# Optimization experiments

Hardware: AMD Instinct MI355X
Metric: run time of the kernel (lower is better)

## Reference

```python
import jax, jax.numpy as jnp
import numpy as np

D_MODEL = 1024
H = 16
DK = 64
DV = 64
EPS = 1e-5


def setup_inputs() -> dict:
    key = jax.random.key(0)
    ks = jax.random.split(key, 12)
    B, NQ, NK = 4, 2048, 2048
    std = 0.001  # init.normal_(weight, std=0.001), biases zero
    return {
        "queries": jax.random.normal(ks[0], (B, NQ, D_MODEL), jnp.float32),
        "keys": jax.random.normal(ks[1], (B, NK, D_MODEL), jnp.float32),
        "values": jax.random.normal(ks[2], (B, NK, D_MODEL), jnp.float32),
        "attention_mask": jnp.ones((B, NK), jnp.int32),  # 1 = keep
        "Wq": jax.random.normal(ks[3], (D_MODEL, H * DK), jnp.float32) * std,
        "bq": jnp.zeros((H * DK,), jnp.float32),
        "Wk": jax.random.normal(ks[4], (D_MODEL, H * DK), jnp.float32) * std,
        "bk": jnp.zeros((H * DK,), jnp.float32),
        "Wv": jax.random.normal(ks[5], (D_MODEL, H * DV), jnp.float32) * std,
        "bv": jnp.zeros((H * DV,), jnp.float32),
        "Wo": jax.random.normal(ks[6], (H * DV, D_MODEL), jnp.float32) * std,
        "bo": jnp.zeros((D_MODEL,), jnp.float32),
        "gamma": jnp.ones((D_MODEL,), jnp.float32),
        "beta": jnp.zeros((D_MODEL,), jnp.float32),
    }


def reference(queries, keys, values, attention_mask, Wq, bq, Wk, bk, Wv, bv, Wo, bo, gamma, beta):
    b, nq, _ = queries.shape
    nk = keys.shape[1]
    q = (queries @ Wq + bq).reshape(b, nq, H, DK)   # (b, nq, h, dk)
    k = (keys @ Wk + bk).reshape(b, nk, H, DK)      # (b, nk, h, dk)
    v = (values @ Wv + bv).reshape(b, nk, H, DV)    # (b, nk, h, dv)
    scale = 1.0 / np.sqrt(DK).astype(np.float32)
    att = jnp.einsum('bqhd,bkhd->bhqk', q, k) * scale  # (b, h, nq, nk)
    mask = attention_mask[:, None, None, :].astype(bool)
    att = jnp.where(mask, att, -jnp.inf)
    att = jax.nn.softmax(att, axis=-1)
    # dropout is identity at inference
    out = jnp.einsum('bhqk,bkhd->bqhd', att, v).reshape(b, nq, H * DV)
    out = out @ Wo + bo
    x = out + queries  # residual
    mean = jnp.mean(x, axis=-1, keepdims=True)
    var = jnp.mean(jnp.square(x - mean), axis=-1, keepdims=True)
    return gamma * (x - mean) * jax.lax.rsqrt(var + EPS) + beta
```

## Files before the change

### kernel.cpp

```cpp
#include <hip/hip_runtime.h>

typedef __bf16 bf16x8 __attribute__((ext_vector_type(8)));
typedef __bf16 bf16x4 __attribute__((ext_vector_type(4)));
typedef float f32x4 __attribute__((ext_vector_type(4)));
typedef unsigned short u16;

#if __has_builtin(__builtin_amdgcn_exp2f)
#define EXP2(x) __builtin_amdgcn_exp2f(x)
#else
#define EXP2(x) exp2f(x)
#endif

__device__ __forceinline__ float bf2f(u16 u){
    union { unsigned int i; float f; } x; x.i = ((unsigned int)u) << 16; return x.f;
}
__device__ __forceinline__ u16 f2bf(float f){
    union { float f; unsigned int i; } x; x.f = f;
    unsigned int r = x.i + 0x7fff + ((x.i >> 16) & 1);
    return (u16)(r >> 16);
}
__device__ __forceinline__ int4 cvt8(const float4 a, const float4 b){
    union { u16 h[8]; int4 v; } u;
    u.h[0] = f2bf(a.x); u.h[1] = f2bf(a.y); u.h[2] = f2bf(a.z); u.h[3] = f2bf(a.w);
    u.h[4] = f2bf(b.x); u.h[5] = f2bf(b.y); u.h[6] = f2bf(b.z); u.h[7] = f2bf(b.w);
    return u.v;
}
__device__ __forceinline__ void gload_lds16(const void* g, void* l){
    __builtin_amdgcn_global_load_lds(
        (const __attribute__((address_space(1))) unsigned int*)g,
        (__attribute__((address_space(3))) unsigned int*)l, 16, 0, 0);
}

__global__ __launch_bounds__(256) void transpose4(
    const float* __restrict__ w0, const float* __restrict__ w1,
    const float* __restrict__ w2, const float* __restrict__ w3,
    u16* __restrict__ out)
{
    __shared__ float tile[32][33];
    int mat = blockIdx.z;
    const float* in = (mat == 0) ? w0 : (mat == 1) ? w1 : (mat == 2) ? w2 : w3;
    u16* o = out + (size_t)mat * 1048576;
    int bx = blockIdx.x * 32, by = blockIdx.y * 32;
    int tx = threadIdx.x & 31, ty = threadIdx.x >> 5;
    #pragma unroll
    for (int i = 0; i < 32; i += 8)
        tile[ty + i][tx] = in[(size_t)(by + ty + i) * 1024 + bx + tx];
    __syncthreads();
    #pragma unroll
    for (int i = 0; i < 32; i += 8)
        o[(size_t)(bx + ty + i) * 1024 + by + tx] = f2bf(tile[tx][ty + i]);
}

template<int MODE, bool AF32>
__global__ __launch_bounds__(256) void gemm_bt(
    const void* __restrict__ Av, const u16* __restrict__ Bt,
    const float* __restrict__ bias, const float* __restrict__ resid,
    void* __restrict__ Cv, float scale)
{
    constexpr int K = 1024;
    __shared__ alignas(16) u16 As[2][128][32];
    __shared__ alignas(16) u16 Bs[2][128][32];
    const int tid = threadIdx.x;
    const int lane = tid & 63, wid = tid >> 6;
    const int wm = wid >> 1, wn = wid & 1;
    const int m0 = blockIdx.x * 128, n0 = blockIdx.y * 128;
    const int r0 = tid >> 2;
    const int kc = (tid & 3) * 8;
    const int fr = lane & 15, fk = (lane >> 4) * 8;

    const float* Af0 = (const float*)Av + (size_t)(m0 + r0) * K + kc;
    const float* Af1 = Af0 + (size_t)64 * K;
    const u16*   Ah0 = (const u16*)Av + (size_t)(m0 + r0) * K + kc;
    const u16*   Ah1 = Ah0 + (size_t)64 * K;
    const u16* Brow0 = Bt + (size_t)(n0 + r0) * K + kc;
    const u16* Brow1 = Brow0 + (size_t)64 * K;

    int4 pa0, pa1, pb0, pb1;
    if constexpr (AF32) {
        pa0 = cvt8(((const float4*)Af0)[0], ((const float4*)Af0)[1]);
        pa1 = cvt8(((const float4*)Af1)[0], ((const float4*)Af1)[1]);
    } else {
        pa0 = *(const int4*)(Ah0);
        pa1 = *(const int4*)(Ah1);
    }
    pb0 = *(const int4*)(Brow0);
    pb1 = *(const int4*)(Brow1);
    *(int4*)&As[0][r0][kc]      = pa0;
    *(int4*)&As[0][r0 + 64][kc] = pa1;
    *(int4*)&Bs[0][r0][kc]      = pb0;
    *(int4*)&Bs[0][r0 + 64][kc] = pb1;
    __syncthreads();

    f32x4 acc[4][4] = {};
    constexpr int NT = K / 32;
    for (int t = 0; t < NT; ++t) {
        int cur = t & 1, nxt = cur ^ 1;
        if (t + 1 < NT) {
            if constexpr (AF32) {
                pa0 = cvt8(((const float4*)(Af0 + (t + 1) * 32))[0],
                           ((const float4*)(Af0 + (t + 1) * 32))[1]);
                pa1 = cvt8(((const float4*)(Af1 + (t + 1) * 32))[0],
                           ((const float4*)(Af1 + (t + 1) * 32))[1]);
            } else {
                pa0 = *(const int4*)(Ah0 + (t + 1) * 32);
                pa1 = *(const int4*)(Ah1 + (t + 1) * 32);
            }
            pb0 = *(const int4*)(Brow0 + (t + 1) * 32);
            pb1 = *(const int4*)(Brow1 + (t + 1) * 32);
        }
        bf16x8 af[4], bfr[4];
        #pragma unroll
        for (int i = 0; i < 4; i++) {
            af[i]  = *(const bf16x8*)&As[cur][wm * 64 + i * 16 + fr][fk];
            bfr[i] = *(const bf16x8*)&Bs[cur][wn * 64 + i * 16 + fr][fk];
        }
        #pragma unroll
        for (int mi = 0; mi < 4; mi++)
            #pragma unroll
            for (int ni = 0; ni < 4; ni++)
                acc[mi][ni] = __builtin_amdgcn_mfma_f32_16x16x32_bf16(
                    af[mi], bfr[ni], acc[mi][ni], 0, 0, 0);
        if (t + 1 < NT) {
            *(int4*)&As[nxt][r0][kc]      = pa0;
            *(int4*)&As[nxt][r0 + 64][kc] = pa1;
            *(int4*)&Bs[nxt][r0][kc]      = pb0;
            *(int4*)&Bs[nxt][r0 + 64][kc] = pb1;
        }
        __syncthreads();
    }

    #pragma unroll
    for (int ni = 0; ni < 4; ni++) {
        int col = n0 + wn * 64 + ni * 16 + fr;
        float bcol = bias[col];
        #pragma unroll
        for (int mi = 0; mi < 4; mi++) {
            #pragma unroll
            for (int r = 0; r < 4; r++) {
                int m = m0 + wm * 64 + mi * 16 + (lane >> 4) * 4 + r;
                float val = acc[mi][ni][r] + bcol;
                if (MODE == 2) {
                    val += resid[(size_t)m * 1024 + col];
                    ((u16*)Cv)[(size_t)m * 1024 + col] = f2bf(val);
                } else {
                    val *= scale;
                    int b = m >> 11, q = m & 2047;
                    int h = col >> 6, d = col & 63;
                    size_t base = (size_t)(b * 16 + h) * 131072;
                    if (MODE == 0) ((u16*)Cv)[base + (size_t)q * 64 + d] = f2bf(val);
                    else           ((u16*)Cv)[base + (size_t)d * 2048 + q] = f2bf(val);
                }
            }
        }
    }
}

__global__ __launch_bounds__(256, 4) void attn_k(
    const u16* __restrict__ Qp, const u16* __restrict__ Kp,
    const u16* __restrict__ Vt, const int* __restrict__ mask,
    u16* __restrict__ O)
{
    __shared__ alignas(16) u16 Ks[2][64][64];
    __shared__ alignas(16) u16 Vs[2][64][64];
    __shared__ alignas(16) u16 Pl[4][16][64];

    const int wg = blockIdx.x;
    const int xc = wg & 7;
    const int rm = wg >> 3;
    const int qx = rm & 15;
    const int bh = (rm >> 4) * 8 + xc;
    const int b = bh >> 4, h = bh & 15;
    const int q0 = qx * 128;
    const int tid = threadIdx.x, wid = tid >> 6, lane = tid & 63;
    const int ql = lane & 15, g = lane >> 4;
    const int qw = q0 + wid * 32;

    const u16* Qbh = Qp + (size_t)bh * 131072;
    const u16* Kbh = Kp + (size_t)bh * 131072;
    const u16* Vbh = Vt + (size_t)bh * 131072;
    const int* mrow = mask + b * 2048;

    char* KsB0 = (char*)Ks;
    char* VsB0 = (char*)Vs;
    char* PlB = (char*)Pl + wid * 2048;

    bf16x8 qf[2][2];
    #pragma unroll
    for (int fi = 0; fi < 2; fi++)
        #pragma unroll
        for (int ks = 0; ks < 2; ks++)
            qf[fi][ks] = *(const bf16x8*)&Qbh[(size_t)(qw + fi * 16 + ql) * 64 + ks * 32 + g * 8];

    f32x4 oacc[2][4] = {};
    float lrow[2] = {0.f, 0.f};
    const f32x4 kZero = {0.f, 0.f, 0.f, 0.f};

    int pwoff[4], proff[2];
    #pragma unroll
    for (int kb = 0; kb < 4; kb++)
        pwoff[kb] = ql * 128 + ((kb * 32 + g * 8) ^ ((ql & 7) << 4));
    #pragma unroll
    for (int ks = 0; ks < 2; ks++)
        proff[ks] = ql * 128 + ((ks * 64 + g * 16) ^ ((ql & 7) << 4));

    const int lrow8 = lane >> 3;
    const int coff  = ((lane & 7) ^ lrow8) << 4;
    const int rb    = wid * 16;

    auto stage = [&](int buf, int tt) {
        const size_t kv0 = (size_t)tt * 64;
        #pragma unroll
        for (int i = 0; i < 2; i++) {
            const int rt = rb + i * 8;
            gload_lds16((const char*)Kbh + (kv0 + rt + lrow8) * 128 + coff,
                        KsB0 + buf * 8192 + rt * 128);
            gload_lds16((const char*)Vbh + (size_t)(rt + lrow8) * 4096 + kv0 * 2 + coff,
                        VsB0 + buf * 8192 + rt * 128);
        }
    };

    stage(0, 0);
    int mcur = mrow[lane];
    __syncthreads();

    for (int t = 0; t < 32; ++t) {
        const int cur = t & 1, nxt = cur ^ 1;
        char* KsB = KsB0 + cur * 8192;
        char* VsB = VsB0 + cur * 8192;
        int mnxt = 1;
        if (t < 31) {
            stage(nxt, t + 1);
            mnxt = mrow[(t + 1) * 64 + lane];
        }
        const bool anym = (__ballot(mcur == 0) != 0ull);

        bf16x8 pf[2][2];
        #pragma unroll
        for (int fi = 0; fi < 2; fi++) {
            float ts = 0.f;
            __builtin_amdgcn_s_setprio(1);
            #pragma unroll
            for (int kb = 0; kb < 4; kb++) {
                const int row = kb * 16 + ql;
                const int swz = (row & 7) << 4;
                bf16x8 kf0 = *(const bf16x8*)(KsB + row * 128 + ((g * 16) ^ swz));
                bf16x8 kf1 = *(const bf16x8*)(KsB + row * 128 + ((64 + g * 16) ^ swz));
                f32x4 a = __builtin_amdgcn_mfma_f32_16x16x32_bf16(kf0, qf[fi][0], kZero, 0, 0, 0);
                a = __builtin_amdgcn_mfma_f32_16x16x32_bf16(kf1, qf[fi][1], a, 0, 0, 0);
                if (anym) {
                    int4 mi = *(const int4*)&mrow[t * 64 + kb * 16 + g * 4];
                    a[0] += mi.x ? 0.f : -1e30f;
                    a[1] += mi.y ? 0.f : -1e30f;
                    a[2] += mi.z ? 0.f : -1e30f;
                    a[3] += mi.w ? 0.f : -1e30f;
                }
                float p0 = EXP2(a[0]);
                float p1 = EXP2(a[1]);
                float p2 = EXP2(a[2]);
                float p3 = EXP2(a[3]);
                ts += (p0 + p1) + (p2 + p3);
                bf16x4 pb;
                pb[0] = (__bf16)p0; pb[1] = (__bf16)p1;
                pb[2] = (__bf16)p2; pb[3] = (__bf16)p3;
                *(bf16x4*)(PlB + pwoff[kb]) = pb;
            }
            __builtin_amdgcn_s_setprio(0);
            lrow[fi] += ts;
            pf[fi][0] = *(const bf16x8*)(PlB + proff[0]);
            pf[fi][1] = *(const bf16x8*)(PlB + proff[1]);
        }

        __builtin_amdgcn_s_setprio(1);
        #pragma unroll
        for (int dt = 0; dt < 4; dt++) {
            int row = dt * 16 + ql;
            int swz = (row & 7) << 4;
            bf16x8 vf0 = *(const bf16x8*)(VsB + row * 128 + ((g * 16) ^ swz));
            bf16x8 vf1 = *(const bf16x8*)(VsB + row * 128 + ((64 + g * 16) ^ swz));
            #pragma unroll
            for (int fi = 0; fi < 2; fi++) {
                oacc[fi][dt] = __builtin_amdgcn_mfma_f32_16x16x32_bf16(vf0, pf[fi][0], oacc[fi][dt], 0, 0, 0);
                oacc[fi][dt] = __builtin_amdgcn_mfma_f32_16x16x32_bf16(vf1, pf[fi][1], oacc[fi][dt], 0, 0, 0);
            }
        }
        __builtin_amdgcn_s_setprio(0);

        mcur = mnxt;
        __syncthreads();
    }

    #pragma unroll
    for (int fi = 0; fi < 2; fi++) {
        lrow[fi] += __shfl_xor(lrow[fi], 16, 64);
        lrow[fi] += __shfl_xor(lrow[fi], 32, 64);
        float inv = 1.f / lrow[fi];
        #pragma unroll
        for (int dt = 0; dt < 4; dt++) {
            bf16x4 ob;
            ob[0] = (__bf16)(oacc[fi][dt][0] * inv);
            ob[1] = (__bf16)(oacc[fi][dt][1] * inv);
            ob[2] = (__bf16)(oacc[fi][dt][2] * inv);
            ob[3] = (__bf16)(oacc[fi][dt][3] * inv);
            *(bf16x4*)(PlB + ql * 128 + ((dt * 32 + g * 8) ^ ((ql & 7) << 4))) = ob;
        }
        int rr = lane >> 2;
        int q = qw + fi * 16 + rr;
        #pragma unroll
        for (int pass = 0; pass < 2; pass++) {
            int cc = (lane & 3) + pass * 4;
            int4 val = *(const int4*)(PlB + rr * 128 + ((cc * 16) ^ ((rr & 7) << 4)));
            *(int4*)&O[((size_t)(b * 2048 + q)) * 1024 + h * 64 + cc * 8] = val;
        }
    }
}

__global__ __launch_bounds__(256) void ln_k(
    const u16* __restrict__ X, const float* __restrict__ gamma,
    const float* __restrict__ beta, float* __restrict__ out)
{
    const int row = blockIdx.x, tid = threadIdx.x;
    ushort4 u = ((const ushort4*)(X + (size_t)row * 1024))[tid];
    float v0 = bf2f(u.x), v1 = bf2f(u.y), v2 = bf2f(u.z), v3 = bf2f(u.w);
    float s = (v0 + v1) + (v2 + v3);
    float s2 = (v0 * v0 + v1 * v1) + (v2 * v2 + v3 * v3);
    #pragma unroll
    for (int off = 1; off < 64; off <<= 1) {
        s  += __shfl_xor(s, off, 64);
        s2 += __shfl_xor(s2, off, 64);
    }
    __shared__ float ss[4], ss2[4];
    int wid = tid >> 6;
    if ((tid & 63) == 0) { ss[wid] = s; ss2[wid] = s2; }
    __syncthreads();
    s = ss[0] + ss[1] + ss[2] + ss[3];
    s2 = ss2[0] + ss2[1] + ss2[2] + ss2[3];
    float mean = s * (1.f / 1024.f);
    float var = s2 * (1.f / 1024.f) - mean * mean;
    float rstd = rsqrtf(var + 1e-5f);
    float4 gm = ((const float4*)gamma)[tid];
    float4 be = ((const float4*)beta)[tid];
    float4 o;
    o.x = (v0 - mean) * rstd * gm.x + be.x;
    o.y = (v1 - mean) * rstd * gm.y + be.y;
    o.z = (v2 - mean) * rstd * gm.z + be.z;
    o.w = (v3 - mean) * rstd * gm.w + be.w;
    ((float4*)(out + (size_t)row * 1024))[tid] = o;
}

extern "C" void kernel_launch(void* const* d_in, const int* in_sizes, int n_in,
                              void* d_out, int out_size, void* d_ws, size_t ws_size,
                              hipStream_t stream)
{
    const float* queries = (const float*)d_in[0];
    const float* keys    = (const float*)d_in[1];
    const float* values  = (const float*)d_in[2];
    const int*   mask    = (const int*)d_in[3];
    const float* Wq = (const float*)d_in[4];
    const float* bq = (const float*)d_in[5];
    const float* Wk = (const float*)d_in[6];
    const float* bk = (const float*)d_in[7];
    const float* Wv = (const float*)d_in[8];
    const float* bv = (const float*)d_in[9];
    const float* Wo = (const float*)d_in[10];
    const float* bo = (const float*)d_in[11];
    const float* gamma = (const float*)d_in[12];
    const float* beta  = (const float*)d_in[13];

    u16* ws = (u16*)d_ws;
    u16* Wt = ws;
    u16* Qp = ws + 4 * 1048576;
    u16* Kp = Qp + 8388608;
    u16* Vt = Kp + 8388608;
    u16* O  = Vt + 8388608;
    u16* X  = Qp;

    const float qscale = 0.125f * 1.44269504088896f;

    transpose4<<<dim3(32, 32, 4), 256, 0, stream>>>(Wq, Wk, Wv, Wo, Wt);
    gemm_bt<0, true ><<<dim3(64, 8), 256, 0, stream>>>(queries, Wt,           bq, nullptr, Qp, qscale);
    gemm_bt<0, true ><<<dim3(64, 8), 256, 0, stream>>>(keys,    Wt + 1048576, bk, nullptr, Kp, 1.0f);
    gemm_bt<1, true ><<<dim3(64, 8), 256, 0, stream>>>(values,  Wt + 2097152, bv, nullptr, Vt, 1.0f);
    attn_k<<<dim3(1024), 256, 0, stream>>>(Qp, Kp, Vt, mask, O);
    gemm_bt<2, false><<<dim3(64, 8), 256, 0, stream>>>(O, Wt + 3145728, bo, queries, X, 1.0f);
    ln_k<<<8192, 256, 0, stream>>>(X, gamma, beta, (float*)d_out);
}
```

Before: 238.6 us.

## Use direct global-to-LDS loads, swizzled LDS, XCD tile mapping and staged epilogue stores in GEMMs

The projection GEMMs now stage B (and bf16 A) tiles with direct global-to-LDS loads into XOR-swizzled shared memory instead of going through registers. Blocks are remapped over a 1D grid so that tiles sharing the same A rows land on the same XCD. The epilogue writes results into a swizzled LDS tile and then emits 16-byte vectorized global stores, including for the transposed V layout. The aim is to cut register staging, LDS bank conflicts and scattered 2-byte global stores. The cost is added swizzle arithmetic and an extra barrier plus LDS pass in the epilogue. gload_lds16 is assumed to be defined in code not shown.

```diff
diff --git a/kernel.cpp b/kernel.cpp
--- a/kernel.cpp
+++ b/kernel.cpp
@@ -58,61 +58,86 @@
     void* __restrict__ Cv, float scale)
 {
     constexpr int K = 1024;
-    __shared__ alignas(16) u16 As[2][128][32];
-    __shared__ alignas(16) u16 Bs[2][128][32];
+    __shared__ alignas(16) u16 smem[16384];
+    char* const AB = (char*)smem;
+    auto Abase = [&](int buf){ return AB + buf * 8192; };
+    auto Bbase = [&](int buf){ return AB + 16384 + buf * 8192; };
+
     const int tid = threadIdx.x;
     const int lane = tid & 63, wid = tid >> 6;
     const int wm = wid >> 1, wn = wid & 1;
-    const int m0 = blockIdx.x * 128, n0 = blockIdx.y * 128;
+
+    const int wg = blockIdx.x;
+    const int xcd = wg & 7, rest = wg >> 3;
+    const int ntile = rest & 7, mhi = rest >> 3;
+    const int m0 = (mhi * 8 + xcd) * 128;
+    const int n0 = ntile * 128;
+
     const int r0 = tid >> 2;
     const int kc = (tid & 3) * 8;
-    const int fr = lane & 15, fk = (lane >> 4) * 8;
+    const int kcB = (tid & 3) * 16;
+    const int fr = lane & 15;
+    const int fkB = (lane >> 4) * 16;
 
     const float* Af0 = (const float*)Av + (size_t)(m0 + r0) * K + kc;
     const float* Af1 = Af0 + (size_t)64 * K;
-    const u16*   Ah0 = (const u16*)Av + (size_t)(m0 + r0) * K + kc;
-    const u16*   Ah1 = Ah0 + (size_t)64 * K;
-    const u16* Brow0 = Bt + (size_t)(n0 + r0) * K + kc;
-    const u16* Brow1 = Brow0 + (size_t)64 * K;
-
-    int4 pa0, pa1, pb0, pb1;
+    const u16*   Ah  = (const u16*)Av;
+
+    const int srow = lane >> 2;
+    auto stageB = [&](int buf, int tcol) {
+        #pragma unroll
+        for (int i = 0; i < 2; i++) {
+            int rt = wid * 32 + i * 16;
+            int r = rt + srow;
+            gload_lds16(Bt + (size_t)(n0 + r) * K + tcol + ((lane & 3) ^ (r & 3)) * 8,
+                        Bbase(buf) + rt * 64);
+        }
+    };
+    auto stageA16 = [&](int buf, int tcol) {
+        #pragma unroll
+        for (int i = 0; i < 2; i++) {
+            int rt = wid * 32 + i * 16;
+            int r = rt + srow;
+            gload_lds16(Ah + (size_t)(m0 + r) * K + tcol + ((lane & 3) ^ (r & 3)) * 8,
+                        Abase(buf) + rt * 64);
+        }
+    };
+    const int aswz = ((r0 & 3) << 4);
+
+    stageB(0, 0);
     if constexpr (AF32) {
-        pa0 = cvt8(((const float4*)Af0)[0], ((const float4*)Af0)[1]);
-        pa1 = cvt8(((const float4*)Af1)[0], ((const float4*)Af1)[1]);
+        int4 w0 = cvt8(((const float4*)Af0)[0], ((const float4*)Af0)[1]);
+        int4 w1 = cvt8(((const float4*)Af1)[0], ((const float4*)Af1)[1]);
+        *(int4*)(Abase(0) + r0 * 64 + (kcB ^ aswz)) = w0;
+        *(int4*)(Abase(0) + (r0 + 64) * 64 + (kcB ^ aswz)) = w1;
     } else {
-        pa0 = *(const int4*)(Ah0);
-        pa1 = *(const int4*)(Ah1);
-    }
-    pb0 = *(const int4*)(Brow0);
-    pb1 = *(const int4*)(Brow1);
-    *(int4*)&As[0][r0][kc]      = pa0;
-    *(int4*)&As[0][r0 + 64][kc] = pa1;
-    *(int4*)&Bs[0][r0][kc]      = pb0;
-    *(int4*)&Bs[0][r0 + 64][kc] = pb1;
+        stageA16(0, 0);
+    }
     __syncthreads();
 
     f32x4 acc[4][4] = {};
     constexpr int NT = K / 32;
     for (int t = 0; t < NT; ++t) {
-        int cur = t & 1, nxt = cur ^ 1;
+        const int cur = t & 1, nxt = cur ^ 1;
+        float4 a00, a01, a10, a11;
         if (t + 1 < NT) {
+            stageB(nxt, (t + 1) * 32);
             if constexpr (AF32) {
-                pa0 = cvt8(((const float4*)(Af0 + (t + 1) * 32))[0],
-                           ((const float4*)(Af0 + (t + 1) * 32))[1]);
-                pa1 = cvt8(((const float4*)(Af1 + (t + 1) * 32))[0],
-                           ((const float4*)(Af1 + (t + 1) * 32))[1]);
+                a00 = ((const float4*)(Af0 + (t + 1) * 32))[0];
+                a01 = ((const float4*)(Af0 + (t + 1) * 32))[1];
+                a10 = ((const float4*)(Af1 + (t + 1) * 32))[0];
+                a11 = ((const float4*)(Af1 + (t + 1) * 32))[1];
             } else {
-                pa0 = *(const int4*)(Ah0 + (t + 1) * 32);
-                pa1 = *(const int4*)(Ah1 + (t + 1) * 32);
+                stageA16(nxt, (t + 1) * 32);
             }
-            pb0 = *(const int4*)(Brow0 + (t + 1) * 32);
-            pb1 = *(const int4*)(Brow1 + (t + 1) * 32);
         }
         bf16x8 af[4], bfr[4];
         #pragma unroll
         for (int i = 0; i < 4; i++) {
-            af[i]  = *(const bf16x8*)&As[cur][wm * 64 + i * 16 + fr][fk];
-            bfr[i] = *(const bf16x8*)&Bs[cur][wn * 64 + i * 16 + fr][fk];
+            int ra = wm * 64 + i * 16 + fr;
+            int rb = wn * 64 + i * 16 + fr;
+            af[i]  = *(const bf16x8*)(Abase(cur) + ra * 64 + (fkB ^ ((ra & 3) << 4)));
+            bfr[i] = *(const bf16x8*)(Bbase(cur) + rb * 64 + (fkB ^ ((rb & 3) << 4)));
         }
         #pragma unroll
         for (int mi = 0; mi < 4; mi++)
@@ -121,36 +146,51 @@
                 acc[mi][ni] = __builtin_amdgcn_mfma_f32_16x16x32_bf16(
                     af[mi], bfr[ni], acc[mi][ni], 0, 0, 0);
         if (t + 1 < NT) {
-            *(int4*)&As[nxt][r0][kc]      = pa0;
-            *(int4*)&As[nxt][r0 + 64][kc] = pa1;
-            *(int4*)&Bs[nxt][r0][kc]      = pb0;
-            *(int4*)&Bs[nxt][r0 + 64][kc] = pb1;
+            if constexpr (AF32) {
+                *(int4*)(Abase(nxt) + r0 * 64 + (kcB ^ aswz)) = cvt8(a00, a01);
+                *(int4*)(Abase(nxt) + (r0 + 64) * 64 + (kcB ^ aswz)) = cvt8(a10, a11);
+            }
         }
         __syncthreads();
     }
 
+    char* const CtB = AB;
     #pragma unroll
     for (int ni = 0; ni < 4; ni++) {
-        int col = n0 + wn * 64 + ni * 16 + fr;
-        float bcol = bias[col];
+        int nn = wn * 64 + ni * 16 + fr;
+        float bcol = bias[n0 + nn];
         #pragma unroll
         for (int mi = 0; mi < 4; mi++) {
             #pragma unroll
             for (int r = 0; r < 4; r++) {
-                int m = m0 + wm * 64 + mi * 16 + (lane >> 4) * 4 + r;
+                int mm = wm * 64 + mi * 16 + (lane >> 4) * 4 + r;
                 float val = acc[mi][ni][r] + bcol;
-                if (MODE == 2) {
-                    val += resid[(size_t)m * 1024 + col];
-                    ((u16*)Cv)[(size_t)m * 1024 + col] = f2bf(val);
-                } else {
-                    val *= scale;
-                    int b = m >> 11, q = m & 2047;
-                    int h = col >> 6, d = col & 63;
-                    size_t base = (size_t)(b * 16 + h) * 131072;
-                    if (MODE == 0) ((u16*)Cv)[base + (size_t)q * 64 + d] = f2bf(val);
-                    else           ((u16*)Cv)[base + (size_t)d * 2048 + q] = f2bf(val);
-                }
+                if (MODE == 2) val += resid[(size_t)(m0 + mm) * 1024 + n0 + nn];
+                else val *= scale;
+                int row  = (MODE == 1) ? nn : mm;
+                int colb = ((MODE == 1) ? mm : nn) * 2;
+                *(u16*)(CtB + row * 256 +
+                        ((colb & 15) | ((((colb >> 4)) ^ (row & 7)) << 4))) = f2bf(val);
             }
+        }
+    }
+    __syncthreads();
+    #pragma unroll
+    for (int p = 0; p < 8; p++) {
+        int idx = p * 256 + tid;
+        int row = idx >> 4, ck = idx & 15;
+        int4 val = *(const int4*)(CtB + row * 256 + ((ck ^ (row & 7)) << 4));
+        if (MODE == 1) {
+            int n = n0 + row, m = m0 + ck * 8;
+            int h = n >> 6, d = n & 63, bb = m >> 11, q = m & 2047;
+            *(int4*)&((u16*)Cv)[(size_t)(bb * 16 + h) * 131072 + (size_t)d * 2048 + q] = val;
+        } else if (MODE == 0) {
+            int m = m0 + row, n = n0 + ck * 8;
+            int h = n >> 6, d = n & 63, bb = m >> 11, q = m & 2047;
+            *(int4*)&((u16*)Cv)[(size_t)(bb * 16 + h) * 131072 + (size_t)q * 64 + d] = val;
+        } else {
+            int m = m0 + row, n = n0 + ck * 8;
+            *(int4*)&((u16*)Cv)[(size_t)m * 1024 + n] = val;
         }
     }
 }
@@ -377,10 +417,10 @@
     const float qscale = 0.125f * 1.44269504088896f;
 
     transpose4<<<dim3(32, 32, 4), 256, 0, stream>>>(Wq, Wk, Wv, Wo, Wt);
-    gemm_bt<0, true ><<<dim3(64, 8), 256, 0, stream>>>(queries, Wt,           bq, nullptr, Qp, qscale);
-    gemm_bt<0, true ><<<dim3(64, 8), 256, 0, stream>>>(keys,    Wt + 1048576, bk, nullptr, Kp, 1.0f);
-    gemm_bt<1, true ><<<dim3(64, 8), 256, 0, stream>>>(values,  Wt + 2097152, bv, nullptr, Vt, 1.0f);
+    gemm_bt<0, true ><<<dim3(512), 256, 0, stream>>>(queries, Wt,           bq, nullptr, Qp, qscale);
+    gemm_bt<0, true ><<<dim3(512), 256, 0, stream>>>(keys,    Wt + 1048576, bk, nullptr, Kp, 1.0f);
+    gemm_bt<1, true ><<<dim3(512), 256, 0, stream>>>(values,  Wt + 2097152, bv, nullptr, Vt, 1.0f);
     attn_k<<<dim3(1024), 256, 0, stream>>>(Qp, Kp, Vt, mask, O);
-    gemm_bt<2, false><<<dim3(64, 8), 256, 0, stream>>>(O, Wt + 3145728, bo, queries, X, 1.0f);
+    gemm_bt<2, false><<<dim3(512), 256, 0, stream>>>(O, Wt + 3145728, bo, queries, X, 1.0f);
     ln_k<<<8192, 256, 0, stream>>>(X, gamma, beta, (float*)d_out);
 }
```

Result: no change. 237.7 us (-0.4%).
